# Performance work log

Hardware: AMD Instinct MI355X
Metric: run time of the kernel (lower is better)

Reference implementation:

```python
import jax, jax.numpy as jnp
import numpy as np

B_SZ, T, P, D, S = 8, 16, 256, 1024, 1024


def setup_inputs() -> dict:
    key = jax.random.key(0)
    ks = jax.random.split(key, 9)
    x = jax.random.normal(ks[0], (B_SZ, T * P, D), dtype=jnp.float32)
    pos_embedding = jax.random.normal(ks[1], (1, T * P, D), dtype=jnp.float32)
    W_in = jax.random.normal(ks[2], (S, D), dtype=jnp.float32) * 0.02
    b_in = jnp.zeros((S,), dtype=jnp.float32)
    W_out = jax.random.normal(ks[3], (D, S), dtype=jnp.float32) * 0.02
    b_out = jnp.zeros((D,), dtype=jnp.float32)
    A = jax.random.normal(ks[4], (S, S), dtype=jnp.float32) * 0.01
    Bm = jax.random.normal(ks[5], (S, S), dtype=jnp.float32) * 0.01
    initial_state = jax.random.normal(ks[6], (1, S), dtype=jnp.float32) * 0.01
    return {"x": x, "pos_embedding": pos_embedding, "W_in": W_in, "b_in": b_in,
            "W_out": W_out, "b_out": b_out, "A": A, "Bm": Bm,
            "initial_state": initial_state}


def reference(x, pos_embedding, W_in, b_in, W_out, b_out, A, Bm, initial_state):
    b, n, d = x.shape
    # add positional embedding (dropout p=0 -> identity)
    x = x + pos_embedding[:, :n]
    x = x.reshape(b, T, P, d)
    # input projection for all frames at once: (b,t,p,s)
    proj = jnp.einsum('btpd,sd->btps', x, W_in) + b_in
    state0 = jnp.broadcast_to(initial_state, (b, S))

    def step(state, proj_t):
        # einsum('sd,bps->bpd', A, state_expanded) == (state @ A) broadcast over p
        # einsum('sd,bps->bpd', B, proj_t)          == proj_t @ B
        state_next = (state @ A)[:, None, :] + proj_t @ Bm  # (b,p,s)
        return state_next.mean(axis=1), state_next

    _, states = jax.lax.scan(step, state0, jnp.swapaxes(proj, 0, 1))  # (t,b,p,s)
    states = jnp.swapaxes(states, 0, 1)  # (b,t,p,s)
    out = jnp.einsum('btps,ds->btpd', states, W_out) + b_out
    return out.reshape(b, T * P, d)
```

## Files before the change

### kernel.cpp

```cpp
#include <hip/hip_runtime.h>
#include <hip/hip_bf16.h>
#include <stdint.h>

typedef __bf16  bf16x8 __attribute__((ext_vector_type(8)));
typedef __bf16  bf16x4 __attribute__((ext_vector_type(4)));
typedef float   f32x4  __attribute__((ext_vector_type(4)));

#define BSZ   8
#define TT    16
#define PP    256
#define DD    1024
#define SS    1024
#define MROWS (BSZ * TT * PP)

__device__ __forceinline__ void gload16(const void* g, void* l) {
    __builtin_amdgcn_global_load_lds(
        (const __attribute__((address_space(1))) void*)g,
        (__attribute__((address_space(3))) void*)l,
        16, 0, 0);
}

__global__ __launch_bounds__(256) void k_xp_mean(const float* __restrict__ x,
                                                 const float* __restrict__ pos,
                                                 __bf16* __restrict__ xp,
                                                 float* __restrict__ part) {
    const int  blk = blockIdx.x;
    const int  c0  = threadIdx.x * 4;
    const long r0  = (long)blk * 32;
    float s0 = 0.f, s1 = 0.f, s2 = 0.f, s3 = 0.f;
#pragma unroll 2
    for (int r = 0; r < 32; ++r) {
        long row = r0 + r;
        long xi  = row * 1024 + c0;
        long pi  = (row & 4095) * 1024 + c0;
        float4 a = *(const float4*)(x + xi);
        float4 p = *(const float4*)(pos + pi);
        float v0 = a.x + p.x, v1 = a.y + p.y, v2 = a.z + p.z, v3 = a.w + p.w;
        bf16x4 o; o[0] = (__bf16)v0; o[1] = (__bf16)v1; o[2] = (__bf16)v2; o[3] = (__bf16)v3;
        *(bf16x4*)(xp + xi) = o;
        s0 += v0; s1 += v1; s2 += v2; s3 += v3;
    }
    float4 s = {s0, s1, s2, s3};
    *(float4*)(part + (long)blk * 1024 + c0) = s;
}

__global__ __launch_bounds__(256) void k_pmean(const float* __restrict__ part,
                                               float* __restrict__ xpm) {
    int idx = blockIdx.x * 256 + threadIdx.x;
    int g = idx >> 10, c = idx & 1023;
    const float* p = part + (long)g * 8192 + c;
    float s = 0.f;
#pragma unroll
    for (int j = 0; j < 8; ++j) s += p[j * 1024];
    xpm[idx] = s * (1.0f / 256.0f);
}

__global__ __launch_bounds__(256) void k_cast(const float* __restrict__ in,
                                              __bf16* __restrict__ out, int n) {
    int i = (blockIdx.x * blockDim.x + threadIdx.x) * 8;
    if (i >= n) return;
    float4 a = *(const float4*)(in + i);
    float4 b = *(const float4*)(in + i + 4);
    bf16x8 o;
    o[0] = (__bf16)a.x; o[1] = (__bf16)a.y; o[2] = (__bf16)a.z; o[3] = (__bf16)a.w;
    o[4] = (__bf16)b.x; o[5] = (__bf16)b.y; o[6] = (__bf16)b.z; o[7] = (__bf16)b.w;
    *(bf16x8*)(out + i) = o;
}

__global__ void k_transpose_bf(const float* __restrict__ in, __bf16* __restrict__ out) {
    __shared__ float tile[32][33];
    int x = blockIdx.x * 32 + threadIdx.x;
    int y = blockIdx.y * 32 + threadIdx.y;
    tile[threadIdx.y][threadIdx.x] = in[(long)y * 1024 + x];
    __syncthreads();
    int ox = blockIdx.y * 32 + threadIdx.x;
    int oy = blockIdx.x * 32 + threadIdx.y;
    out[(long)oy * 1024 + ox] = (__bf16)tile[threadIdx.x][threadIdx.y];
}

__global__ void k_transpose_f32(const float* __restrict__ in, float* __restrict__ out) {
    __shared__ float tile[32][33];
    int x = blockIdx.x * 32 + threadIdx.x;
    int y = blockIdx.y * 32 + threadIdx.y;
    tile[threadIdx.y][threadIdx.x] = in[(long)y * 1024 + x];
    __syncthreads();
    int ox = blockIdx.y * 32 + threadIdx.x;
    int oy = blockIdx.x * 32 + threadIdx.y;
    out[(long)oy * 1024 + ox] = tile[threadIdx.x][threadIdx.y];
}

template <int EPI>
__global__ __launch_bounds__(256) void gemm_nt(const __bf16* __restrict__ A,
                                               const __bf16* __restrict__ B,
                                               void* __restrict__ Cout,
                                               const float* __restrict__ VO) {
    constexpr int K = 1024;
    const int tid  = threadIdx.x;
    const int lane = tid & 63;
    const int w    = tid >> 6;
    const int wr   = w >> 1, wc = w & 1;
    const long bm  = (long)blockIdx.x * 128;
    const long bn  = (long)blockIdx.y * 128;

    __shared__ __bf16 As[128 * 64];
    __shared__ __bf16 Bs[128 * 64];

    f32x4 acc[4][4];
#pragma unroll
    for (int i = 0; i < 4; ++i)
#pragma unroll
        for (int j = 0; j < 4; ++j) acc[i][j] = (f32x4){0.f, 0.f, 0.f, 0.f};

    const int sr = (w << 3) + (lane >> 3);
    const int sc = (lane & 7) << 3;
    const __bf16* Ap = A + (bm + sr) * K + sc;
    const __bf16* Bp = B + (bn + sr) * K + sc;

    for (int kt = 0; kt < K; kt += 64) {
        if (kt) __syncthreads();
#pragma unroll
        for (int j = 0; j < 4; ++j) {
            gload16(Ap + (long)j * 32 * K + kt, &As[j * 2048 + w * 512]);
            gload16(Bp + (long)j * 32 * K + kt, &Bs[j * 2048 + w * 512]);
        }
        __syncthreads();

#pragma unroll
        for (int kk = 0; kk < 2; ++kk) {
            const int ko = kk * 32 + ((lane >> 4) << 3);
            bf16x8 af[4], bfr[4];
#pragma unroll
            for (int i = 0; i < 4; ++i) {
                int ar = wr * 64 + i * 16 + (lane & 15);
                af[i]  = *(const bf16x8*)&As[ar * 64 + ko];
                int br = wc * 64 + i * 16 + (lane & 15);
                bfr[i] = *(const bf16x8*)&Bs[br * 64 + ko];
            }
#pragma unroll
            for (int mi = 0; mi < 4; ++mi)
#pragma unroll
                for (int ni = 0; ni < 4; ++ni)
                    acc[mi][ni] = __builtin_amdgcn_mfma_f32_16x16x32_bf16(
                        af[mi], bfr[ni], acc[mi][ni], 0, 0, 0);
        }
    }

    const int r0 = (lane >> 4) << 2;
    const int c0 = lane & 15;
#pragma unroll
    for (int mi = 0; mi < 4; ++mi) {
#pragma unroll
        for (int ni = 0; ni < 4; ++ni) {
#pragma unroll
            for (int j = 0; j < 4; ++j) {
                long gm = bm + wr * 64 + mi * 16 + r0 + j;
                long gn = bn + wc * 64 + ni * 16 + c0;
                float val = acc[mi][ni][j];
                if constexpr (EPI == 1) {
                    ((__bf16*)Cout)[gm * 1024 + gn] = (__bf16)val;
                } else {
                    ((float*)Cout)[gm * 1024 + gn] = val + VO[(gm >> 8) * 1024 + gn];
                }
            }
        }
    }
}

template <int BIAS>
__global__ __launch_bounds__(256) void small_nt(const float* __restrict__ A,
                                                const float* __restrict__ B,
                                                float* __restrict__ C,
                                                const float* __restrict__ bias1,
                                                const float* __restrict__ bias2) {
    __shared__ float Asm[8][1024];
    __shared__ float Red[128][8];
    const int m0  = blockIdx.x * 8;
    const int n0  = blockIdx.y * 128;
    const int tid = threadIdx.x;
#pragma unroll
    for (int j = 0; j < 8; ++j) {
        int fi = j * 1024 + tid * 4;
        *(float4*)(&Asm[0][0] + fi) = *(const float4*)(A + (long)m0 * 1024 + fi);
    }
    __syncthreads();
    const int n  = n0 + (tid & 127);
    const int kh = tid >> 7;
    float p[8];
#pragma unroll
    for (int m = 0; m < 8; ++m) p[m] = 0.f;
    const float* Bp = B + (long)n * 1024 + kh * 512;
    for (int k = 0; k < 512; k += 4) {
        float4 bv = *(const float4*)(Bp + k);
        int kk = kh * 512 + k;
#pragma unroll
        for (int m = 0; m < 8; ++m)
            p[m] += Asm[m][kk] * bv.x + Asm[m][kk + 1] * bv.y +
                    Asm[m][kk + 2] * bv.z + Asm[m][kk + 3] * bv.w;
    }
    if (kh) {
#pragma unroll
        for (int m = 0; m < 8; ++m) Red[tid & 127][m] = p[m];
    }
    __syncthreads();
    if (!kh) {
#pragma unroll
        for (int m = 0; m < 8; ++m) {
            float vv = p[m] + Red[tid][m];
            if (BIAS >= 1) vv += bias1[n];
            if (BIAS >= 2) vv += bias2[n];
            C[(long)(m0 + m) * 1024 + n] = vv;
        }
    }
}

__global__ __launch_bounds__(256) void k_bb(const __bf16* __restrict__ BWT,
                                            const float* __restrict__ b_in,
                                            float* __restrict__ bb) {
    int d    = blockIdx.x * 4 + (threadIdx.x >> 6);
    int lane = threadIdx.x & 63;
    const __bf16* row = BWT + (long)d * 1024 + lane * 16;
    float acc = 0.f;
#pragma unroll
    for (int i = 0; i < 2; ++i) {
        bf16x8 v = *(const bf16x8*)(row + i * 8);
        const float* bi = b_in + lane * 16 + i * 8;
#pragma unroll
        for (int j = 0; j < 8; ++j) acc += (float)v[j] * bi[j];
    }
#pragma unroll
    for (int off = 32; off; off >>= 1) acc += __shfl_xor(acc, off);
    if (!lane) bb[d] = acc;
}

__global__ __launch_bounds__(256) void k_init_state(const float* __restrict__ init,
                                                    float* __restrict__ state) {
    int idx = blockIdx.x * 256 + threadIdx.x;
    state[idx] = init[idx & 1023];
}

__global__ __launch_bounds__(256) void k_step(const float* __restrict__ AT,
                                              const float* __restrict__ Mbuf,
                                              float* __restrict__ v,
                                              float* __restrict__ state,
                                              int t) {
    int gw   = blockIdx.x * 4 + (threadIdx.x >> 6);
    int b    = gw >> 10;
    int sp   = gw & 1023;
    int lane = threadIdx.x & 63;
    const float* at = AT + (long)sp * 1024 + lane * 16;
    const float* st = state + (t & 1) * 8192 + b * 1024 + lane * 16;
    float acc = 0.f;
#pragma unroll
    for (int i = 0; i < 4; ++i) {
        float4 a = *(const float4*)(at + i * 4);
        float4 s = *(const float4*)(st + i * 4);
        acc += a.x * s.x + a.y * s.y + a.z * s.z + a.w * s.w;
    }
#pragma unroll
    for (int off = 32; off; off >>= 1) acc += __shfl_xor(acc, off);
    if (lane == 0) {
        float vt = acc;
        long bt = (long)b * 16 + t;
        v[bt * 1024 + sp] = vt;
        state[((t + 1) & 1) * 8192 + b * 1024 + sp] = vt + Mbuf[bt * 1024 + sp];
    }
}

extern "C" void kernel_launch(void* const* d_in, const int* in_sizes, int n_in,
                              void* d_out, int out_size, void* d_ws, size_t ws_size,
                              hipStream_t stream) {
    const float* x    = (const float*)d_in[0];
    const float* pos  = (const float*)d_in[1];
    const float* W_in = (const float*)d_in[2];
    const float* b_in = (const float*)d_in[3];
    const float* W_out= (const float*)d_in[4];
    const float* b_out= (const float*)d_in[5];
    const float* A    = (const float*)d_in[6];
    const float* Bm   = (const float*)d_in[7];
    const float* is0  = (const float*)d_in[8];
    float* out = (float*)d_out;

    char* ws = (char*)d_ws;
    const size_t o_XP     = 0;
    const size_t o_Part   = 67108864;
    const size_t o_XPm    = 71303168;
    const size_t o_projM  = 71827456;
    const size_t o_Mbuf   = 72351744;
    const size_t o_v      = 72876032;
    const size_t o_VO     = 73400320;
    const size_t o_state  = 73924608;
    const size_t o_bb     = 73990144;
    const size_t o_AT     = 73994240;
    const size_t o_BmT    = 78188544;
    const size_t o_Wout16 = 82382848;
    const size_t o_Bm16   = 84480000;
    const size_t o_WinT16 = 86577152;
    const size_t o_BWT    = 88674304;
    const size_t o_G      = 90771456;
    const size_t need     = 92868608;
    if (ws_size < need) return;

    __bf16* XP     = (__bf16*)(ws + o_XP);
    float*  Part   = (float*)(ws + o_Part);
    float*  XPm    = (float*)(ws + o_XPm);
    float*  projM  = (float*)(ws + o_projM);
    float*  Mbuf   = (float*)(ws + o_Mbuf);
    float*  v      = (float*)(ws + o_v);
    float*  VO     = (float*)(ws + o_VO);
    float*  state  = (float*)(ws + o_state);
    float*  bb     = (float*)(ws + o_bb);
    float*  AT     = (float*)(ws + o_AT);
    float*  BmT    = (float*)(ws + o_BmT);
    __bf16* Wout16 = (__bf16*)(ws + o_Wout16);
    __bf16* Bm16   = (__bf16*)(ws + o_Bm16);
    __bf16* WinT16 = (__bf16*)(ws + o_WinT16);
    __bf16* BWT    = (__bf16*)(ws + o_BWT);
    __bf16* G      = (__bf16*)(ws + o_G);

    k_cast<<<512, 256, 0, stream>>>(W_out, Wout16, SS * DD);
    k_cast<<<512, 256, 0, stream>>>(Bm, Bm16, SS * SS);
    k_transpose_bf<<<dim3(32, 32), dim3(32, 32), 0, stream>>>(W_in, WinT16);
    k_transpose_f32<<<dim3(32, 32), dim3(32, 32), 0, stream>>>(A, AT);
    k_transpose_f32<<<dim3(32, 32), dim3(32, 32), 0, stream>>>(Bm, BmT);
    k_init_state<<<32, 256, 0, stream>>>(is0, state);

    k_xp_mean<<<1024, 256, 0, stream>>>(x, pos, XP, Part);
    k_pmean<<<512, 256, 0, stream>>>(Part, XPm);

    gemm_nt<1><<<dim3(8, 8), 256, 0, stream>>>(Wout16, Bm16, (void*)BWT, nullptr);
    gemm_nt<1><<<dim3(8, 8), 256, 0, stream>>>(BWT, WinT16, (void*)G, nullptr);
    k_bb<<<256, 256, 0, stream>>>(BWT, b_in, bb);

    small_nt<1><<<dim3(16, 8), 256, 0, stream>>>(XPm, W_in, projM, b_in, nullptr);
    small_nt<0><<<dim3(16, 8), 256, 0, stream>>>(projM, BmT, Mbuf, nullptr, nullptr);

    for (int t = 0; t < 16; ++t)
        k_step<<<2048, 256, 0, stream>>>(AT, Mbuf, v, state, t);

    small_nt<2><<<dim3(16, 8), 256, 0, stream>>>(v, W_out, VO, b_out, bb);

    gemm_nt<2><<<dim3(256, 8), 256, 0, stream>>>(XP, G, (void*)out, VO);
}
```

Baseline: 579.6 us.

## Fuse weight prep kernels, drop Bm transpose, swizzle GEMM block order

Merges the two casts and two transposes into a single prep kernel, which cuts the number of kernel launches. The transpose of Bm is removed by adding a small NN matmul that reads Bm directly. The GEMM now uses a 1D grid with a swizzled block-to-tile mapping so that neighbouring blocks share B tiles, which should improve L2 reuse. The large output GEMM dominates the runtime, so only the swizzle is likely to affect total time noticeably.

```diff
diff --git a/kernel.cpp b/kernel.cpp
--- a/kernel.cpp
+++ b/kernel.cpp
@@ -11,13 +11,54 @@
 #define PP    256
 #define DD    1024
 #define SS    1024
-#define MROWS (BSZ * TT * PP)
 
 __device__ __forceinline__ void gload16(const void* g, void* l) {
     __builtin_amdgcn_global_load_lds(
         (const __attribute__((address_space(1))) void*)g,
         (__attribute__((address_space(3))) void*)l,
         16, 0, 0);
+}
+
+__global__ __launch_bounds__(256) void k_prep(const float* __restrict__ Wout, __bf16* __restrict__ Wout16,
+                                              const float* __restrict__ Bm,   __bf16* __restrict__ Bm16,
+                                              const float* __restrict__ Win,  __bf16* __restrict__ WinT16,
+                                              const float* __restrict__ A,    float* __restrict__ AT) {
+    const int bx = blockIdx.x;
+    if (bx < 1024) {
+        const float* src = (bx < 512) ? Wout : Bm;
+        __bf16* dst = (bx < 512) ? Wout16 : Bm16;
+        int i = ((bx & 511) * 256 + threadIdx.x) * 8;
+        float4 a = *(const float4*)(src + i);
+        float4 b = *(const float4*)(src + i + 4);
+        bf16x8 o;
+        o[0] = (__bf16)a.x; o[1] = (__bf16)a.y; o[2] = (__bf16)a.z; o[3] = (__bf16)a.w;
+        o[4] = (__bf16)b.x; o[5] = (__bf16)b.y; o[6] = (__bf16)b.z; o[7] = (__bf16)b.w;
+        *(bf16x8*)(dst + i) = o;
+    } else if (bx < 2048) {
+        __shared__ float tile[32][33];
+        int tb = bx - 1024;
+        int tx = tb & 31, ty = tb >> 5;
+        int lx = threadIdx.x & 31, ly = threadIdx.x >> 5;
+#pragma unroll
+        for (int r = 0; r < 32; r += 8)
+            tile[ly + r][lx] = Win[(long)(ty * 32 + ly + r) * 1024 + tx * 32 + lx];
+        __syncthreads();
+#pragma unroll
+        for (int r = 0; r < 32; r += 8)
+            WinT16[(long)(tx * 32 + ly + r) * 1024 + ty * 32 + lx] = (__bf16)tile[lx][ly + r];
+    } else {
+        __shared__ float tile[32][33];
+        int tb = bx - 2048;
+        int tx = tb & 31, ty = tb >> 5;
+        int lx = threadIdx.x & 31, ly = threadIdx.x >> 5;
+#pragma unroll
+        for (int r = 0; r < 32; r += 8)
+            tile[ly + r][lx] = A[(long)(ty * 32 + ly + r) * 1024 + tx * 32 + lx];
+        __syncthreads();
+#pragma unroll
+        for (int r = 0; r < 32; r += 8)
+            AT[(long)(tx * 32 + ly + r) * 1024 + ty * 32 + lx] = tile[lx][ly + r];
+    }
 }
 
 __global__ __launch_bounds__(256) void k_xp_mean(const float* __restrict__ x,
@@ -55,40 +96,6 @@
     xpm[idx] = s * (1.0f / 256.0f);
 }
 
-__global__ __launch_bounds__(256) void k_cast(const float* __restrict__ in,
-                                              __bf16* __restrict__ out, int n) {
-    int i = (blockIdx.x * blockDim.x + threadIdx.x) * 8;
-    if (i >= n) return;
-    float4 a = *(const float4*)(in + i);
-    float4 b = *(const float4*)(in + i + 4);
-    bf16x8 o;
-    o[0] = (__bf16)a.x; o[1] = (__bf16)a.y; o[2] = (__bf16)a.z; o[3] = (__bf16)a.w;
-    o[4] = (__bf16)b.x; o[5] = (__bf16)b.y; o[6] = (__bf16)b.z; o[7] = (__bf16)b.w;
-    *(bf16x8*)(out + i) = o;
-}
-
-__global__ void k_transpose_bf(const float* __restrict__ in, __bf16* __restrict__ out) {
-    __shared__ float tile[32][33];
-    int x = blockIdx.x * 32 + threadIdx.x;
-    int y = blockIdx.y * 32 + threadIdx.y;
-    tile[threadIdx.y][threadIdx.x] = in[(long)y * 1024 + x];
-    __syncthreads();
-    int ox = blockIdx.y * 32 + threadIdx.x;
-    int oy = blockIdx.x * 32 + threadIdx.y;
-    out[(long)oy * 1024 + ox] = (__bf16)tile[threadIdx.x][threadIdx.y];
-}
-
-__global__ void k_transpose_f32(const float* __restrict__ in, float* __restrict__ out) {
-    __shared__ float tile[32][33];
-    int x = blockIdx.x * 32 + threadIdx.x;
-    int y = blockIdx.y * 32 + threadIdx.y;
-    tile[threadIdx.y][threadIdx.x] = in[(long)y * 1024 + x];
-    __syncthreads();
-    int ox = blockIdx.y * 32 + threadIdx.x;
-    int oy = blockIdx.x * 32 + threadIdx.y;
-    out[(long)oy * 1024 + ox] = tile[threadIdx.x][threadIdx.y];
-}
-
 template <int EPI>
 __global__ __launch_bounds__(256) void gemm_nt(const __bf16* __restrict__ A,
                                                const __bf16* __restrict__ B,
@@ -99,8 +106,10 @@
     const int lane = tid & 63;
     const int w    = tid >> 6;
     const int wr   = w >> 1, wc = w & 1;
-    const long bm  = (long)blockIdx.x * 128;
-    const long bn  = (long)blockIdx.y * 128;
+    const int cpx = gridDim.x >> 3;
+    const int swz = (blockIdx.x & 7) * cpx + (blockIdx.x >> 3);
+    const long bm = (long)(swz >> 3) * 128;
+    const long bn = (long)(swz & 7) * 128;
 
     __shared__ __bf16 As[128 * 64];
     __shared__ __bf16 Bs[128 * 64];
@@ -210,6 +219,44 @@
             if (BIAS >= 2) vv += bias2[n];
             C[(long)(m0 + m) * 1024 + n] = vv;
         }
+    }
+}
+
+__global__ __launch_bounds__(256) void small_nn(const float* __restrict__ A,
+                                                const float* __restrict__ B,
+                                                float* __restrict__ C) {
+    __shared__ float Asm[8][1024];
+    __shared__ float Red[128][8];
+    const int m0  = blockIdx.x * 8;
+    const int n0  = blockIdx.y * 128;
+    const int tid = threadIdx.x;
+#pragma unroll
+    for (int j = 0; j < 8; ++j) {
+        int fi = j * 1024 + tid * 4;
+        *(float4*)(&Asm[0][0] + fi) = *(const float4*)(A + (long)m0 * 1024 + fi);
+    }
+    __syncthreads();
+    const int n  = n0 + (tid & 127);
+    const int kh = tid >> 7;
+    float p[8];
+#pragma unroll
+    for (int m = 0; m < 8; ++m) p[m] = 0.f;
+    const float* Bp = B + n + (long)kh * 512 * 1024;
+    for (int k = 0; k < 512; ++k) {
+        float bv = Bp[(long)k * 1024];
+        int kk = kh * 512 + k;
+#pragma unroll
+        for (int m = 0; m < 8; ++m) p[m] += Asm[m][kk] * bv;
+    }
+    if (kh) {
+#pragma unroll
+        for (int m = 0; m < 8; ++m) Red[tid & 127][m] = p[m];
+    }
+    __syncthreads();
+    if (!kh) {
+#pragma unroll
+        for (int m = 0; m < 8; ++m)
+            C[(long)(m0 + m) * 1024 + n] = p[m] + Red[tid][m];
     }
 }
 
@@ -288,16 +335,15 @@
     const size_t o_Mbuf   = 72351744;
     const size_t o_v      = 72876032;
     const size_t o_VO     = 73400320;
-    const size_t o_state  = 73924608;
-    const size_t o_bb     = 73990144;
-    const size_t o_AT     = 73994240;
-    const size_t o_BmT    = 78188544;
-    const size_t o_Wout16 = 82382848;
-    const size_t o_Bm16   = 84480000;
-    const size_t o_WinT16 = 86577152;
-    const size_t o_BWT    = 88674304;
-    const size_t o_G      = 90771456;
-    const size_t need     = 92868608;
+    const size_t o_bb     = 73924608;
+    const size_t o_state  = 73990144;
+    const size_t o_AT     = 74055680;
+    const size_t o_Wout16 = 78249984;
+    const size_t o_Bm16   = 80347136;
+    const size_t o_WinT16 = 82444288;
+    const size_t o_BWT    = 84541440;
+    const size_t o_G      = 86638592;
+    const size_t need     = 88735744;
     if (ws_size < need) return;
 
     __bf16* XP     = (__bf16*)(ws + o_XP);
@@ -307,37 +353,26 @@
     float*  Mbuf   = (float*)(ws + o_Mbuf);
     float*  v      = (float*)(ws + o_v);
     float*  VO     = (float*)(ws + o_VO);
+    float*  bb     = (float*)(ws + o_bb);
     float*  state  = (float*)(ws + o_state);
-    float*  bb     = (float*)(ws + o_bb);
     float*  AT     = (float*)(ws + o_AT);
-    float*  BmT    = (float*)(ws + o_BmT);
     __bf16* Wout16 = (__bf16*)(ws + o_Wout16);
     __bf16* Bm16   = (__bf16*)(ws + o_Bm16);
     __bf16* WinT16 = (__bf16*)(ws + o_WinT16);
     __bf16* BWT    = (__bf16*)(ws + o_BWT);
     __bf16* G      = (__bf16*)(ws + o_G);
 
-    k_cast<<<512, 256, 0, stream>>>(W_out, Wout16, SS * DD);
-    k_cast<<<512, 256, 0, stream>>>(Bm, Bm16, SS * SS);
-    k_transpose_bf<<<dim3(32, 32), dim3(32, 32), 0, stream>>>(W_in, WinT16);
-    k_transpose_f32<<<dim3(32, 32), dim3(32, 32), 0, stream>>>(A, AT);
-    k_transpose_f32<<<dim3(32, 32), dim3(32, 32), 0, stream>>>(Bm, BmT);
-    k_init_state<<<32, 256, 0, stream>>>(is0, state);
-
+    k_prep<<<3072, 256, 0, stream>>>(W_out, Wout16, Bm, Bm16, W_in, WinT16, A, AT);
     k_xp_mean<<<1024, 256, 0, stream>>>(x, pos, XP, Part);
     k_pmean<<<512, 256, 0, stream>>>(Part, XPm);
-
-    gemm_nt<1><<<dim3(8, 8), 256, 0, stream>>>(Wout16, Bm16, (void*)BWT, nullptr);
-    gemm_nt<1><<<dim3(8, 8), 256, 0, stream>>>(BWT, WinT16, (void*)G, nullptr);
+    gemm_nt<1><<<64, 256, 0, stream>>>(Wout16, Bm16, (void*)BWT, nullptr);
+    gemm_nt<1><<<64, 256, 0, stream>>>(BWT, WinT16, (void*)G, nullptr);
     k_bb<<<256, 256, 0, stream>>>(BWT, b_in, bb);
-
     small_nt<1><<<dim3(16, 8), 256, 0, stream>>>(XPm, W_in, projM, b_in, nullptr);
-    small_nt<0><<<dim3(16, 8), 256, 0, stream>>>(projM, BmT, Mbuf, nullptr, nullptr);
-
+    small_nn<<<dim3(16, 8), 256, 0, stream>>>(projM, Bm, Mbuf);
+    k_init_state<<<32, 256, 0, stream>>>(is0, state);
     for (int t = 0; t < 16; ++t)
         k_step<<<2048, 256, 0, stream>>>(AT, Mbuf, v, state, t);
-
     small_nt<2><<<dim3(16, 8), 256, 0, stream>>>(v, W_out, VO, b_out, bb);
-
-    gemm_nt<2><<<dim3(256, 8), 256, 0, stream>>>(XP, G, (void*)out, VO);
-}
+    gemm_nt<2><<<2048, 256, 0, stream>>>(XP, G, (void*)out, VO);
+}
```

After: 575.5 us. About the same (-0.7%).
